# Kernel optimization log

Hardware: AMD Instinct MI355X
Metric: run time of the kernel (lower is better)

## Reference

```python
import jax, jax.numpy as jnp
import numpy as np
import math

SUN = 9.0            # global SuN constant in the repo (sudoku N=9)
TB = 16              # t-block size for L1-score computation (bounds peak memory)


def quick_gelu(x):
    return x * jax.nn.sigmoid(1.702 * x)


def l1_scores(q, k):
    # q, k: (b, t, h, d)  ->  scores (b, h, t, s) = -sum_d |q[b,t,h,:] - k[b,s,h,:]|
    # Blocked over t so we never materialize the full (b,t,s,h,d) tensor.
    b, t, h, d = q.shape
    nb = t // TB
    qb = q.reshape(b, nb, TB, h, d).swapaxes(0, 1)  # (nb, b, TB, h, d)

    def blk(carry, qi):
        # qi: (b, TB, h, d); diff block: (b, TB, s, h, d) -> (b, TB, s, h)
        s = -jnp.sum(jnp.abs(qi[:, :, None, :, :] - k[:, None, :, :, :]), axis=-1)
        return carry, s

    _, out = jax.lax.scan(blk, None, qb)            # (nb, b, TB, s, h)
    out = out.transpose(1, 0, 2, 3, 4).reshape(b, t, t, h)  # (b, t, s, h)
    return out.transpose(0, 3, 1, 2)                # (b, h, t, s)


def setup_inputs() -> dict:
    key = jax.random.key(0)
    ks = jax.random.split(key, 5)
    b, t, d, h = 8, 512, 128, 8
    x = jax.random.normal(ks[0], (b, t, d), dtype=jnp.float32)
    msk = jax.random.uniform(ks[1], (1, h, t, t), dtype=jnp.float32)
    # LinearM(d_model, n_head*2*d_model): w is (outdim, indim+1), uniform*scl, bias col zeroed
    scl_qv = math.sqrt(6.0) / math.sqrt(d + h * 2 * d)
    wqv_w = jax.random.uniform(ks[2], (h * 2 * d, d + 1), dtype=jnp.float32) * scl_qv
    wqv_w = wqv_w.at[:, -1].set(0.0)
    # LinearNobias(d_model, n_head): w is (n_head, d_model); used directly as per-head k-gate
    scl_k = math.sqrt(6.0) / math.sqrt(d + h)
    wk_w = jax.random.uniform(ks[3], (h, d), dtype=jnp.float32) * scl_k
    # fanout = LinearM(d_model, d_model)
    scl_f = math.sqrt(6.0) / math.sqrt(2 * d)
    fanout_w = jax.random.uniform(ks[4], (d, d + 1), dtype=jnp.float32) * scl_f
    fanout_w = fanout_w.at[:, -1].set(0.0)
    return {"x": x, "msk": msk, "wqv_w": wqv_w, "wk_w": wk_w, "fanout_w": fanout_w}


def reference(x, msk, wqv_w, wk_w, fanout_w):
    b, t, d = x.shape
    h = wk_w.shape[0]
    # wqv: LinearM -> (b, t, h*2*d)
    y = jnp.einsum('oi,bti->bto', wqv_w[:, :-1], x) + wqv_w[:, -1]
    y = y.reshape(b, t, h, 2 * d)
    q, v = y[..., :d], y[..., d:]                      # each (b, t, h, d)
    # k = x expanded per head, gated elementwise by wk.w (per-head, per-dim gate)
    k = x[:, :, None, :] * wk_w[None, None, :, :]      # (b, t, h, d)
    # gv gate: all heads enabled (init_zeros=False) -> identity multiply on v
    a = l1_scores(q, k) / math.sqrt(d)                 # (b, h, t, s)
    a = jax.nn.softmax(a, axis=3) * msk                # mask AFTER softmax (as in source)
    # combine + sum over heads: einsum('bhts,bshd->bthd') then sum(dim=2 of bthd == h)
    bo = jnp.einsum('bhts,bshd->btd', a, v)            # (b, t, d)
    yo = quick_gelu(bo + SUN / 2.0) - SUN / 2.0
    yo = jnp.einsum('oi,bti->bto', fanout_w[:, :-1], yo) + fanout_w[:, -1]
    return x + yo
```

## Files before the change

kernel.cpp:

```cpp
#include <hip/hip_runtime.h>
#include <hip/hip_bf16.h>
#include <math.h>

#define BB 8
#define TT 512
#define DD 128
#define HH 8
#define OO 2048
#define WCOLS 129
#define SCALE 0.08838834764831845f
#define IT 16
#define SC2 64
#define NC (TT / SC2)
#define Q8SCL 32.0f
#define Q8OFF 128.0f
#define SCALE_Q8 (SCALE / Q8SCL)

typedef __attribute__((ext_vector_type(8))) short short8;
typedef __attribute__((ext_vector_type(4))) float floatx4;

static __device__ __forceinline__ float bf2f(__hip_bfloat16 v) { return __bfloat162float(v); }
static __device__ __forceinline__ float us2f(unsigned short u) {
  union { unsigned int i; float f; } cv; cv.i = ((unsigned int)u) << 16; return cv.f;
}
static __device__ __forceinline__ unsigned short f2us(float f) {
  union { float f; unsigned int i; } cv; cv.f = f;
  unsigned int lsb = (cv.i >> 16) & 1u;
  return (unsigned short)((cv.i + 0x7fffu + lsb) >> 16);
}
static __device__ __forceinline__ float ldin(const void* p, int i, int isf) {
  return isf ? ((const float*)p)[i] : bf2f(((const __hip_bfloat16*)p)[i]);
}
static __device__ __forceinline__ unsigned char quant8(float v) {
  float f = fminf(fmaxf(v * Q8SCL + Q8OFF, 0.0f), 255.0f);
  return (unsigned char)(f + 0.5f);
}
static __device__ __forceinline__ int detect_isf(const void* x) {
  const unsigned int* w = (const unsigned int*)x;
  int cnt = 0;
#pragma unroll
  for (int i = 0; i < 64; ++i) {
    float a = fabsf(us2f((unsigned short)(w[i] & 0xFFFFu)));
    cnt += (a > 0.05f && a < 8.0f) ? 1 : 0;
  }
  return (cnt < 32) ? 1 : 0;
}

#if __has_builtin(__builtin_amdgcn_sad_u8)
#define SAD8(a, b, c) __builtin_amdgcn_sad_u8((a), (b), (c))
#elif __has_builtin(__builtin_amdgcn_sad_u16)
static __device__ __forceinline__ unsigned int SAD8(unsigned int a, unsigned int b, unsigned int c) {
  unsigned int alo = a & 0x00FF00FFu, ahi = (a >> 8) & 0x00FF00FFu;
  unsigned int blo = b & 0x00FF00FFu, bhi = (b >> 8) & 0x00FF00FFu;
  c = __builtin_amdgcn_sad_u16(alo, blo, c);
  return __builtin_amdgcn_sad_u16(ahi, bhi, c);
}
#else
static __device__ __forceinline__ unsigned int SAD8(unsigned int a, unsigned int b, unsigned int c) {
#pragma unroll
  for (int i = 0; i < 4; ++i) {
    int d = (int)((a >> (8 * i)) & 0xFF) - (int)((b >> (8 * i)) & 0xFF);
    c += (unsigned int)(d < 0 ? -d : d);
  }
  return c;
}
#endif

__global__ void k_prep(const void* __restrict__ x,
                       const void* __restrict__ wqv,
                       const void* __restrict__ wk,
                       const void* __restrict__ fo,
                       float* __restrict__ qvb,
                       float* __restrict__ foT, float* __restrict__ fob,
                       float* __restrict__ wkf,
                       unsigned short* __restrict__ wqvb,
                       unsigned short* __restrict__ xb,
                       int* __restrict__ flg) {
  int isf = detect_isf(x);
  int stride = gridDim.x * blockDim.x;
  int idx = blockIdx.x * blockDim.x + threadIdx.x;
  if (idx == 0) *flg = isf;
  for (int i = idx; i < OO * DD; i += stride) {
    int o = i >> 7, ii = i & 127;
    wqvb[i] = f2us(ldin(wqv, o * WCOLS + ii, isf));
  }
  for (int o = idx; o < OO; o += stride) qvb[o] = ldin(wqv, o * WCOLS + DD, isf);
  for (int i = idx; i < DD * DD; i += stride) {
    int o = i & (DD - 1), ii = i >> 7;
    foT[i] = ldin(fo, o * WCOLS + ii, isf);
  }
  for (int o = idx; o < DD; o += stride) fob[o] = ldin(fo, o * WCOLS + DD, isf);
  for (int i = idx; i < HH * DD; i += stride) wkf[i] = ldin(wk, i, isf);
  {
    int n4 = BB * TT * DD / 4;
    for (int i4 = idx; i4 < n4; i4 += stride) {
      if (isf) {
        float4 f = ((const float4*)x)[i4];
        unsigned int lo = (unsigned int)f2us(f.x) | ((unsigned int)f2us(f.y) << 16);
        unsigned int hi = (unsigned int)f2us(f.z) | ((unsigned int)f2us(f.w) << 16);
        uint2 o2; o2.x = lo; o2.y = hi;
        ((uint2*)xb)[i4] = o2;
      } else {
        ((uint2*)xb)[i4] = ((const uint2*)x)[i4];
      }
    }
  }
}

__global__ __launch_bounds__(256) void k_qvm(const unsigned short* __restrict__ xb,
                                             const unsigned short* __restrict__ wqvb,
                                             const float* __restrict__ qvb,
                                             unsigned char* __restrict__ q2b,
                                             unsigned short* __restrict__ vt) {
  __shared__ __align__(16) unsigned short xs[32][136];
  __shared__ __align__(16) unsigned short vtile[128][40];
  __shared__ __align__(16) unsigned char qtile[32][144];
  int rb = blockIdx.x * 32;
  int cb = blockIdx.y * 256;
  int tid = threadIdx.x;
#pragma unroll
  for (int p = 0; p < 2; ++p) {
    int e = tid + p * 256;
    int row = e >> 4, c16 = e & 15;
    *(uint4*)&xs[row][c16 * 8] = *(const uint4*)&xb[(size_t)(rb + row) * DD + c16 * 8];
  }
  __syncthreads();
  int lane = tid & 63;
  int w = tid >> 6;
  int mI = lane & 15;
  int quad = lane >> 4;
  int cw = cb + w * 64;
  floatx4 acc[2][4];
#pragma unroll
  for (int rt = 0; rt < 2; ++rt)
#pragma unroll
    for (int ct = 0; ct < 4; ++ct) acc[rt][ct] = (floatx4){0.f, 0.f, 0.f, 0.f};
#pragma unroll
  for (int j = 0; j < 4; ++j) {
    short8 av[2], bv[4];
#pragma unroll
    for (int rt = 0; rt < 2; ++rt)
      av[rt] = *(const short8*)&xs[rt * 16 + mI][j * 32 + quad * 8];
#pragma unroll
    for (int ct = 0; ct < 4; ++ct)
      bv[ct] = *(const short8*)&wqvb[(size_t)(cw + ct * 16 + mI) * DD + j * 32 + quad * 8];
#pragma unroll
    for (int rt = 0; rt < 2; ++rt)
#pragma unroll
      for (int ct = 0; ct < 4; ++ct)
        acc[rt][ct] = __builtin_amdgcn_mfma_f32_16x16x32_bf16(av[rt], bv[ct], acc[rt][ct], 0, 0, 0);
  }
#pragma unroll
  for (int rt = 0; rt < 2; ++rt) {
#pragma unroll
    for (int ct = 0; ct < 4; ++ct) {
      int o = cw + ct * 16 + mI;
      float bias = qvb[o];
      int cc = o & 255;
#pragma unroll
      for (int reg = 0; reg < 4; ++reg) {
        int r = rb + rt * 16 + quad * 4 + reg;
        float val = acc[rt][ct][reg] + bias;
        if (cc < DD) qtile[r - rb][cc] = quant8(val);
        else         vtile[cc - DD][r - rb] = f2us(val);
      }
    }
  }
  __syncthreads();
  {
    int b = rb >> 9, t0 = rb & 511;
    int h = cb >> 8;
    {
      int row = tid >> 3, c16 = (tid & 7) * 16;
      unsigned char* qdst = q2b + ((size_t)(b * HH + h) * TT + t0 + row) * DD + c16;
      *(uint4*)qdst = *(const uint4*)&qtile[row][c16];
    }
    {
      int n = tid >> 1, half = tid & 1;
      unsigned short* dst = vt + (((size_t)(b * HH + h) * DD) + n) * TT + t0 + half * 16;
      uint4 a0 = *(const uint4*)&vtile[n][half * 16];
      uint4 a1 = *(const uint4*)&vtile[n][half * 16 + 8];
      *(uint4*)&dst[0] = a0;
      *(uint4*)&dst[8] = a1;
    }
  }
}

__global__ __launch_bounds__(256) void k_k(const unsigned short* __restrict__ xb,
                                           const float* __restrict__ wkf,
                                           unsigned char* __restrict__ ku8) {
  int gid = blockIdx.x * 256 + threadIdx.x;
  int d0 = (gid & 7) * 16;
  int s  = (gid >> 3) & 511;
  int h  = (gid >> 12) & 7;
  int b  = gid >> 15;
  const unsigned short* xr = xb + ((size_t)(b * TT + s) * DD) + d0;
  const float* wr = wkf + h * DD + d0;
  uint4 xa = *(const uint4*)&xr[0];
  uint4 xc = *(const uint4*)&xr[8];
  float4 w0 = *(const float4*)&wr[0];
  float4 w1 = *(const float4*)&wr[4];
  float4 w2 = *(const float4*)&wr[8];
  float4 w3 = *(const float4*)&wr[12];
  unsigned char out[16];
  const unsigned int* xw = (const unsigned int*)&xa;
  const unsigned int* yw = (const unsigned int*)&xc;
  const float* wf = (const float*)&w0;
  float wv[16];
  wv[0]=w0.x; wv[1]=w0.y; wv[2]=w0.z; wv[3]=w0.w;
  wv[4]=w1.x; wv[5]=w1.y; wv[6]=w1.z; wv[7]=w1.w;
  wv[8]=w2.x; wv[9]=w2.y; wv[10]=w2.z; wv[11]=w2.w;
  wv[12]=w3.x; wv[13]=w3.y; wv[14]=w3.z; wv[15]=w3.w;
  (void)wf;
#pragma unroll
  for (int j = 0; j < 8; ++j) {
    unsigned int word = (j < 4) ? xw[j] : yw[j - 4];
    float xlo = us2f((unsigned short)(word & 0xFFFFu));
    float xhi = us2f((unsigned short)(word >> 16));
    out[j * 2]     = quant8(xlo * wv[j * 2]);
    out[j * 2 + 1] = quant8(xhi * wv[j * 2 + 1]);
  }
  *(uint4*)(ku8 + (((size_t)(b * HH + h) * TT + s) * DD) + d0) = *(const uint4*)out;
}

static __device__ __forceinline__ void sad_chunk(const unsigned int (*__restrict__ kb)[36],
                                                 const unsigned int (*__restrict__ qp)[36],
                                                 int r0, int r1, int si, int rot,
                                                 float* __restrict__ r, int c) {
  unsigned int a00 = 0, a01 = 0, a10 = 0, a11 = 0;
  const unsigned int* k0r = &kb[2 * si][0];
  const unsigned int* k1r = &kb[2 * si + 1][0];
  const unsigned int* q0r = &qp[r0][0];
  const unsigned int* q1r = &qp[r1][0];
#pragma unroll
  for (int j8 = 0; j8 < 32; j8 += 8) {
    int i0 = (j8 + rot) & 31;
    int i1 = (j8 + rot + 4) & 31;
    uint4 qa0 = *(const uint4*)&q0r[i0];
    uint4 qa1 = *(const uint4*)&q0r[i1];
    uint4 qb0 = *(const uint4*)&q1r[i0];
    uint4 qb1 = *(const uint4*)&q1r[i1];
    uint4 ka0 = *(const uint4*)&k0r[i0];
    uint4 ka1 = *(const uint4*)&k0r[i1];
    uint4 kb0 = *(const uint4*)&k1r[i0];
    uint4 kb1 = *(const uint4*)&k1r[i1];
    a00 = SAD8(qa0.x, ka0.x, a00); a00 = SAD8(qa0.y, ka0.y, a00);
    a00 = SAD8(qa0.z, ka0.z, a00); a00 = SAD8(qa0.w, ka0.w, a00);
    a00 = SAD8(qa1.x, ka1.x, a00); a00 = SAD8(qa1.y, ka1.y, a00);
    a00 = SAD8(qa1.z, ka1.z, a00); a00 = SAD8(qa1.w, ka1.w, a00);
    a01 = SAD8(qa0.x, kb0.x, a01); a01 = SAD8(qa0.y, kb0.y, a01);
    a01 = SAD8(qa0.z, kb0.z, a01); a01 = SAD8(qa0.w, kb0.w, a01);
    a01 = SAD8(qa1.x, kb1.x, a01); a01 = SAD8(qa1.y, kb1.y, a01);
    a01 = SAD8(qa1.z, kb1.z, a01); a01 = SAD8(qa1.w, kb1.w, a01);
    a10 = SAD8(qb0.x, ka0.x, a10); a10 = SAD8(qb0.y, ka0.y, a10);
    a10 = SAD8(qb0.z, ka0.z, a10); a10 = SAD8(qb0.w, ka0.w, a10);
    a10 = SAD8(qb1.x, ka1.x, a10); a10 = SAD8(qb1.y, ka1.y, a10);
    a10 = SAD8(qb1.z, ka1.z, a10); a10 = SAD8(qb1.w, ka1.w, a10);
    a11 = SAD8(qb0.x, kb0.x, a11); a11 = SAD8(qb0.y, kb0.y, a11);
    a11 = SAD8(qb0.z, kb0.z, a11); a11 = SAD8(qb0.w, kb0.w, a11);
    a11 = SAD8(qb1.x, kb1.x, a11); a11 = SAD8(qb1.y, kb1.y, a11);
    a11 = SAD8(qb1.z, kb1.z, a11); a11 = SAD8(qb1.w, kb1.w, a11);
  }
  r[c * 2]          = -(float)a00 * SCALE_Q8;
  r[c * 2 + 1]      = -(float)a01 * SCALE_Q8;
  r[16 + c * 2]     = -(float)a10 * SCALE_Q8;
  r[16 + c * 2 + 1] = -(float)a11 * SCALE_Q8;
}

__global__ __launch_bounds__(256) void k_flash(const void* __restrict__ msk,
                                               const int* __restrict__ flag,
                                               const unsigned char* __restrict__ q2b,
                                               const unsigned char* __restrict__ ku8,
                                               const unsigned short* __restrict__ vt,
                                               unsigned short* __restrict__ yo8) {
  __shared__ __align__(16) unsigned int qp[IT][36];
  __shared__ __align__(16) unsigned int kp[2][SC2][36];
  __shared__ __align__(16) unsigned short ps[IT][TT + 8];
  int isf = *flag;
  int bh = blockIdx.x;
  int h = bh & 7;
  int it0 = blockIdx.y * IT;
  int tid = threadIdx.x;

  const uint4* qrow = (const uint4*)(q2b + ((size_t)bh * TT + it0) * DD);
  if (tid < 128) {
    *(uint4*)&qp[tid >> 3][(tid & 7) * 4] = qrow[tid];
  }

  int ig2 = tid >> 5;
  int si = tid & 31;
  int r0 = ig2 * 2, r1 = r0 + 1;
  int rot = (si & 7) * 4;
  float r[32];

  const uint4* kc4 = (const uint4*)(ku8 + (size_t)bh * TT * DD);
  uint4 kreg[2];
#pragma unroll
  for (int p = 0; p < 2; ++p) kreg[p] = kc4[tid + p * 256];

#pragma unroll
  for (int c = 0; c < NC; ++c) {
    unsigned int (*kb)[36] = kp[c & 1];
#pragma unroll
    for (int p = 0; p < 2; ++p) {
      int e = tid + p * 256;
      *(uint4*)&kb[e >> 3][(e & 7) * 4] = kreg[p];
    }
    if (c < NC - 1) {
#pragma unroll
      for (int p = 0; p < 2; ++p)
        kreg[p] = kc4[(c + 1) * 512 + tid + p * 256];
    }
    __syncthreads();
    sad_chunk(kb, qp, r0, r1, si, rot, r, c);
  }

  float m0 = -1e30f, m1 = -1e30f;
#pragma unroll
  for (int j = 0; j < 16; ++j) { m0 = fmaxf(m0, r[j]); m1 = fmaxf(m1, r[16 + j]); }
#pragma unroll
  for (int off = 16; off; off >>= 1) {
    m0 = fmaxf(m0, __shfl_xor(m0, off, 32));
    m1 = fmaxf(m1, __shfl_xor(m1, off, 32));
  }
  float s0 = 0.f, s1 = 0.f;
#pragma unroll
  for (int j = 0; j < 16; ++j) {
    r[j] = __expf(r[j] - m0);           s0 += r[j];
    r[16 + j] = __expf(r[16 + j] - m1); s1 += r[16 + j];
  }
#pragma unroll
  for (int off = 16; off; off >>= 1) {
    s0 += __shfl_xor(s0, off, 32);
    s1 += __shfl_xor(s1, off, 32);
  }
  float inv0 = 1.0f / s0, inv1 = 1.0f / s1;

  int mb0 = (h * TT + it0 + r0) * TT;
  int mb1 = mb0 + TT;
#pragma unroll
  for (int c = 0; c < NC; ++c) {
    int s = c * SC2 + 2 * si;
    float p00 = r[c * 2]          * inv0 * ldin(msk, mb0 + s, isf);
    float p01 = r[c * 2 + 1]      * inv0 * ldin(msk, mb0 + s + 1, isf);
    float p10 = r[16 + c * 2]     * inv1 * ldin(msk, mb1 + s, isf);
    float p11 = r[16 + c * 2 + 1] * inv1 * ldin(msk, mb1 + s + 1, isf);
    *(unsigned int*)&ps[r0][s] = (unsigned int)f2us(p00) | ((unsigned int)f2us(p01) << 16);
    *(unsigned int*)&ps[r1][s] = (unsigned int)f2us(p10) | ((unsigned int)f2us(p11) << 16);
  }
  __syncthreads();

  {
    int lane = tid & 63;
    int w = tid >> 6;
    int mI = lane & 15;
    int quad = lane >> 4;
    int n0 = w * 32;
    floatx4 acc0 = {0.f, 0.f, 0.f, 0.f};
    floatx4 acc1 = {0.f, 0.f, 0.f, 0.f};
    const unsigned short* vb0 = vt + ((size_t)bh * DD + n0 + mI) * TT;
    const unsigned short* vb1 = vb0 + 16 * TT;
#pragma unroll
    for (int st = 0; st < 4; ++st) {
      short8 av[4], b0v[4], b1v[4];
#pragma unroll
      for (int j = 0; j < 4; ++j) {
        int krow = st * 128 + j * 32 + quad * 8;
        b0v[j] = *(const short8*)&vb0[krow];
        b1v[j] = *(const short8*)&vb1[krow];
        av[j]  = *(const short8*)&ps[mI][krow];
      }
#pragma unroll
      for (int j = 0; j < 4; ++j) {
        acc0 = __builtin_amdgcn_mfma_f32_16x16x32_bf16(av[j], b0v[j], acc0, 0, 0, 0);
        acc1 = __builtin_amdgcn_mfma_f32_16x16x32_bf16(av[j], b1v[j], acc1, 0, 0, 0);
      }
    }
    unsigned short* yb = yo8 + ((size_t)bh * TT + it0) * DD;
#pragma unroll
    for (int reg = 0; reg < 4; ++reg) {
      int row = quad * 4 + reg;
      yb[row * DD + n0 + mI]      = f2us(acc0[reg]);
      yb[row * DD + n0 + 16 + mI] = f2us(acc1[reg]);
    }
  }
}

__global__ __launch_bounds__(256) void k_fanout(const void* __restrict__ x,
                                                const int* __restrict__ flag,
                                                const unsigned short* __restrict__ yo8,
                                                const float* __restrict__ foT,
                                                const float* __restrict__ fob,
                                                void* __restrict__ outv) {
  __shared__ float ys[16][132];
  int isf = *flag;
  int m0 = blockIdx.x * 16;
  int tid = threadIdx.x;
  {
    int mr = tid >> 4;
    int i8 = (tid & 15) * 8;
    int r = m0 + mr;
    int bb = r >> 9, t = r & 511;
    size_t base = ((size_t)bb * HH * TT + t) * DD + i8;
    float s[8] = {0.f, 0.f, 0.f, 0.f, 0.f, 0.f, 0.f, 0.f};
#pragma unroll
    for (int hh = 0; hh < HH; ++hh) {
      short8 v = *(const short8*)&yo8[base + (size_t)hh * TT * DD];
#pragma unroll
      for (int j = 0; j < 8; ++j) s[j] += us2f((unsigned short)v[j]);
    }
#pragma unroll
    for (int j = 0; j < 8; ++j) {
      float z = s[j] + 4.5f;
      ys[mr][i8 + j] = z / (1.0f + __expf(-1.702f * z)) - 4.5f;
    }
  }
  __syncthreads();
  int ty = tid >> 5, tx = tid & 31;
  float acc[2][4] = {};
  for (int ii = 0; ii < 128; ++ii) {
    float4 w4 = *(const float4*)(foT + ii * DD + tx * 4);
    float y0 = ys[ty * 2 + 0][ii], y1 = ys[ty * 2 + 1][ii];
    acc[0][0] += y0 * w4.x; acc[0][1] += y0 * w4.y; acc[0][2] += y0 * w4.z; acc[0][3] += y0 * w4.w;
    acc[1][0] += y1 * w4.x; acc[1][1] += y1 * w4.y; acc[1][2] += y1 * w4.z; acc[1][3] += y1 * w4.w;
  }
#pragma unroll
  for (int rr = 0; rr < 2; ++rr) {
    int r = m0 + ty * 2 + rr;
#pragma unroll
    for (int c = 0; c < 4; ++c) {
      int o = tx * 4 + c;
      float val = acc[rr][c] + fob[o] + ldin(x, r * DD + o, isf);
      if (isf) ((float*)outv)[r * DD + o] = val;
      else     ((__hip_bfloat16*)outv)[r * DD + o] = __float2bfloat16(val);
    }
  }
}

extern "C" void kernel_launch(void* const* d_in, const int* in_sizes, int n_in,
                              void* d_out, int out_size, void* d_ws, size_t ws_size,
                              hipStream_t stream) {
  const void* x   = d_in[0];
  const void* msk = d_in[1];
  const void* wqv = d_in[2];
  const void* wk  = d_in[3];
  const void* fo  = d_in[4];

  float* qvb = (float*)d_ws;
  float* foT = qvb + 2048;
  float* fob = foT + 16384;
  float* wkf = fob + 128;
  int*   flg = (int*)(wkf + 1024);
  unsigned short* wqvb = (unsigned short*)(flg + 16);
  unsigned short* xb   = wqvb + 262144;
  unsigned char*  q2b  = (unsigned char*)(xb + 524288);
  unsigned char*  ku8  = q2b + 4194304;
  unsigned short* v2   = (unsigned short*)(ku8 + 4194304);
  unsigned short* vt   = v2 + 4194304;
  unsigned short* yo8  = v2;

  k_prep<<<256, 256, 0, stream>>>(x, wqv, wk, fo, qvb, foT, fob, wkf, wqvb, xb, flg);
  k_qvm<<<dim3(128, 8), 256, 0, stream>>>(xb, wqvb, qvb, q2b, vt);
  k_k<<<1024, 256, 0, stream>>>(xb, wkf, ku8);
  k_flash<<<dim3(64, 32), 256, 0, stream>>>(msk, flg, q2b, ku8, vt, yo8);
  k_fanout<<<256, 256, 0, stream>>>(x, flg, yo8, foT, fob, d_out);
}
```

Measured before the change: 170.9 us.

## Halve flash-attention row tile to 8 rows with 128-thread blocks

Shrinks the per-block query tile from 16 to 8 rows and launches twice as many 128-thread blocks. The K chunk buffer goes from double- to single-buffered, with an extra barrier per chunk, and each thread now loads four K vectors instead of two. In the PV stage each wave covers 64 output columns with four MFMA accumulators over 8 valid rows, duplicating those rows into the 16-row MFMA tile and writing only half the result. The aim is more blocks and occupancy, at the cost of half-wasted MFMA work, twice the V traffic per output row, and more synchronisation.

```diff
diff --git a/kernel.cpp b/kernel.cpp
--- a/kernel.cpp
+++ b/kernel.cpp
@@ -9,7 +9,7 @@
 #define OO 2048
 #define WCOLS 129
 #define SCALE 0.08838834764831845f
-#define IT 16
+#define IT 8
 #define SC2 64
 #define NC (TT / SC2)
 #define Q8SCL 32.0f
@@ -205,13 +205,11 @@
   unsigned char out[16];
   const unsigned int* xw = (const unsigned int*)&xa;
   const unsigned int* yw = (const unsigned int*)&xc;
-  const float* wf = (const float*)&w0;
   float wv[16];
   wv[0]=w0.x; wv[1]=w0.y; wv[2]=w0.z; wv[3]=w0.w;
   wv[4]=w1.x; wv[5]=w1.y; wv[6]=w1.z; wv[7]=w1.w;
   wv[8]=w2.x; wv[9]=w2.y; wv[10]=w2.z; wv[11]=w2.w;
   wv[12]=w3.x; wv[13]=w3.y; wv[14]=w3.z; wv[15]=w3.w;
-  (void)wf;
 #pragma unroll
   for (int j = 0; j < 8; ++j) {
     unsigned int word = (j < 4) ? xw[j] : yw[j - 4];
@@ -267,14 +265,14 @@
   r[16 + c * 2 + 1] = -(float)a11 * SCALE_Q8;
 }
 
-__global__ __launch_bounds__(256) void k_flash(const void* __restrict__ msk,
+__global__ __launch_bounds__(128) void k_flash(const void* __restrict__ msk,
                                                const int* __restrict__ flag,
                                                const unsigned char* __restrict__ q2b,
                                                const unsigned char* __restrict__ ku8,
                                                const unsigned short* __restrict__ vt,
                                                unsigned short* __restrict__ yo8) {
   __shared__ __align__(16) unsigned int qp[IT][36];
-  __shared__ __align__(16) unsigned int kp[2][SC2][36];
+  __shared__ __align__(16) unsigned int kp[SC2][36];
   __shared__ __align__(16) unsigned short ps[IT][TT + 8];
   int isf = *flag;
   int bh = blockIdx.x;
@@ -283,7 +281,7 @@
   int tid = threadIdx.x;
 
   const uint4* qrow = (const uint4*)(q2b + ((size_t)bh * TT + it0) * DD);
-  if (tid < 128) {
+  if (tid < 64) {
     *(uint4*)&qp[tid >> 3][(tid & 7) * 4] = qrow[tid];
   }
 
@@ -294,25 +292,25 @@
   float r[32];
 
   const uint4* kc4 = (const uint4*)(ku8 + (size_t)bh * TT * DD);
-  uint4 kreg[2];
-#pragma unroll
-  for (int p = 0; p < 2; ++p) kreg[p] = kc4[tid + p * 256];
+  uint4 kreg[4];
+#pragma unroll
+  for (int p = 0; p < 4; ++p) kreg[p] = kc4[tid + p * 128];
 
 #pragma unroll
   for (int c = 0; c < NC; ++c) {
-    unsigned int (*kb)[36] = kp[c & 1];
-#pragma unroll
-    for (int p = 0; p < 2; ++p) {
-      int e = tid + p * 256;
-      *(uint4*)&kb[e >> 3][(e & 7) * 4] = kreg[p];
+    __syncthreads();
+#pragma unroll
+    for (int p = 0; p < 4; ++p) {
+      int e = tid + p * 128;
+      *(uint4*)&kp[e >> 3][(e & 7) * 4] = kreg[p];
     }
     if (c < NC - 1) {
 #pragma unroll
-      for (int p = 0; p < 2; ++p)
-        kreg[p] = kc4[(c + 1) * 512 + tid + p * 256];
+      for (int p = 0; p < 4; ++p)
+        kreg[p] = kc4[(c + 1) * 512 + tid + p * 128];
     }
     __syncthreads();
-    sad_chunk(kb, qp, r0, r1, si, rot, r, c);
+    sad_chunk(kp, qp, r0, r1, si, rot, r, c);
   }
 
   float m0 = -1e30f, m1 = -1e30f;
@@ -355,33 +353,39 @@
     int w = tid >> 6;
     int mI = lane & 15;
     int quad = lane >> 4;
-    int n0 = w * 32;
-    floatx4 acc0 = {0.f, 0.f, 0.f, 0.f};
-    floatx4 acc1 = {0.f, 0.f, 0.f, 0.f};
-    const unsigned short* vb0 = vt + ((size_t)bh * DD + n0 + mI) * TT;
-    const unsigned short* vb1 = vb0 + 16 * TT;
+    int n0 = w * 64;
+    floatx4 acc[4];
+#pragma unroll
+    for (int ct = 0; ct < 4; ++ct) acc[ct] = (floatx4){0.f, 0.f, 0.f, 0.f};
+    const unsigned short* vb[4];
+#pragma unroll
+    for (int ct = 0; ct < 4; ++ct)
+      vb[ct] = vt + ((size_t)bh * DD + n0 + ct * 16 + mI) * TT;
 #pragma unroll
     for (int st = 0; st < 4; ++st) {
-      short8 av[4], b0v[4], b1v[4];
-#pragma unroll
-      for (int j = 0; j < 4; ++j) {
-        int krow = st * 128 + j * 32 + quad * 8;
-        b0v[j] = *(const short8*)&vb0[krow];
-        b1v[j] = *(const short8*)&vb1[krow];
-        av[j]  = *(const short8*)&ps[mI][krow];
+      short8 av[4];
+#pragma unroll
+      for (int j = 0; j < 4; ++j)
+        av[j] = *(const short8*)&ps[mI & 7][st * 128 + j * 32 + quad * 8];
+#pragma unroll
+      for (int ct = 0; ct < 4; ++ct) {
+#pragma unroll
+        for (int j = 0; j < 4; ++j) {
+          short8 bv = *(const short8*)&vb[ct][st * 128 + j * 32 + quad * 8];
+          acc[ct] = __builtin_amdgcn_mfma_f32_16x16x32_bf16(av[j], bv, acc[ct], 0, 0, 0);
+        }
       }
-#pragma unroll
-      for (int j = 0; j < 4; ++j) {
-        acc0 = __builtin_amdgcn_mfma_f32_16x16x32_bf16(av[j], b0v[j], acc0, 0, 0, 0);
-        acc1 = __builtin_amdgcn_mfma_f32_16x16x32_bf16(av[j], b1v[j], acc1, 0, 0, 0);
+    }
+    if (quad < 2) {
+      unsigned short* yb = yo8 + ((size_t)bh * TT + it0) * DD;
+#pragma unroll
+      for (int ct = 0; ct < 4; ++ct) {
+#pragma unroll
+        for (int reg = 0; reg < 4; ++reg) {
+          int row = quad * 4 + reg;
+          yb[row * DD + n0 + ct * 16 + mI] = f2us(acc[ct][reg]);
+        }
       }
-    }
-    unsigned short* yb = yo8 + ((size_t)bh * TT + it0) * DD;
-#pragma unroll
-    for (int reg = 0; reg < 4; ++reg) {
-      int row = quad * 4 + reg;
-      yb[row * DD + n0 + mI]      = f2us(acc0[reg]);
-      yb[row * DD + n0 + 16 + mI] = f2us(acc1[reg]);
     }
   }
 }
@@ -462,6 +466,6 @@
   k_prep<<<256, 256, 0, stream>>>(x, wqv, wk, fo, qvb, foT, fob, wkf, wqvb, xb, flg);
   k_qvm<<<dim3(128, 8), 256, 0, stream>>>(xb, wqvb, qvb, q2b, vt);
   k_k<<<1024, 256, 0, stream>>>(xb, wkf, ku8);
-  k_flash<<<dim3(64, 32), 256, 0, stream>>>(msk, flg, q2b, ku8, vt, yo8);
+  k_flash<<<dim3(64, 64), 128, 0, stream>>>(msk, flg, q2b, ku8, vt, yo8);
   k_fanout<<<256, 256, 0, stream>>>(x, flg, yo8, foT, fob, d_out);
 }
```

New measurement: 233.9 us. 1.37x slower.
